# Performance work log

Measured on AMD Instinct MI355X. Metric: run time of the kernel, lower is better.

The kernel has to match this reference:

```python
import jax, jax.numpy as jnp
import numpy as np

DIV_VAL = 11.313708498984761  # sqrt(128), the softmax temperature used as div_val


def setup_inputs() -> dict:
    key = jax.random.key(0)
    kq, kk, kv = jax.random.split(key, 3)
    B, Lq, Lk, D = 16, 4096, 4096, 128
    return {
        "query": jax.random.normal(kq, (B, Lq, D), dtype=jnp.float32),
        "key": jax.random.normal(kk, (B, Lk, D), dtype=jnp.float32),
        "value": jax.random.normal(kv, (B, Lk, D), dtype=jnp.float32),
    }


def reference(query, key, value):
    # qk = Q @ K^T, scaled by 1/div_val  -> [B, Lq, Lk]
    scaled_qk = jnp.einsum("bqd,bkd->bqk", query, key) / DIV_VAL
    # numerically stable softmax over last axis; dropout is identity (eval / p=0)
    attn = jax.nn.softmax(scaled_qk, axis=-1)
    # output = attn @ V -> [B, Lq, Dv]
    return jnp.einsum("bqk,bkd->bqd", attn, value)
```

## Files before the change

### kernel.cpp

```cpp
#include <hip/hip_runtime.h>

#define B_  16
#define L_  4096
#define D_  128
#define NT  (L_ / 64)

typedef __attribute__((ext_vector_type(8)))  __bf16 bf16x8;
typedef __attribute__((ext_vector_type(2)))  __bf16 bf16x2;
typedef __attribute__((ext_vector_type(16))) float  f32x16;
typedef __attribute__((ext_vector_type(4)))  float  f32x4;
typedef __attribute__((ext_vector_type(4)))  int    i32x4;
typedef __attribute__((ext_vector_type(8)))  unsigned short u16x8;
typedef __attribute__((ext_vector_type(4)))  unsigned short u16x4;

#ifndef __has_builtin
#define __has_builtin(x) 0
#endif
#if __has_builtin(__builtin_amdgcn_permlane32_swap)
#define HAVE_PLSWAP 1
#else
#define HAVE_PLSWAP 0
#endif

__device__ __forceinline__ unsigned short f2bf(float f){
  unsigned u = __builtin_bit_cast(unsigned, f);
  u += 0x7fffu + ((u >> 16) & 1u);
  return (unsigned short)(u >> 16);
}

__device__ __forceinline__ int packbf(float a, float b){
  bf16x2 t; t[0] = (__bf16)a; t[1] = (__bf16)b;
  return __builtin_bit_cast(int, t);
}

__device__ __forceinline__ void gload16(const void* g, void* l){
  __builtin_amdgcn_global_load_lds(
      (const __attribute__((address_space(1))) unsigned int*)g,
      (__attribute__((address_space(3))) unsigned int*)l, 16, 0, 0);
}

__device__ __forceinline__ f32x16 z16(){
  f32x16 t;
#pragma unroll
  for (int i = 0; i < 16; ++i) t[i] = 0.f;
  return t;
}

__global__ void cvt_bf16_kernel(const float* __restrict__ in,
                                unsigned short* __restrict__ out, int n8,
                                float scale){
  int i = blockIdx.x * blockDim.x + threadIdx.x;
  if (i >= n8) return;
  const float4* p = reinterpret_cast<const float4*>(in) + (size_t)i * 2;
  float4 a = p[0], b = p[1];
  u16x8 o;
  o[0]=f2bf(a.x*scale); o[1]=f2bf(a.y*scale); o[2]=f2bf(a.z*scale); o[3]=f2bf(a.w*scale);
  o[4]=f2bf(b.x*scale); o[5]=f2bf(b.y*scale); o[6]=f2bf(b.z*scale); o[7]=f2bf(b.w*scale);
  reinterpret_cast<u16x8*>(out)[i] = o;
}

__global__ void transpose_v_kernel(const float* __restrict__ V,
                                   unsigned short* __restrict__ Vt){
  __shared__ unsigned short tile[64][65];
  const int k0 = blockIdx.x * 64, d0 = blockIdx.y * 64, b = blockIdx.z;
  const int tr = threadIdx.x >> 4, tc = threadIdx.x & 15;
  const float* src = V + ((size_t)b * L_ + k0) * D_ + d0;
#pragma unroll
  for (int p = 0; p < 4; ++p){
    int kl = p * 16 + tr;
    float4 v = *reinterpret_cast<const float4*>(src + (size_t)kl * D_ + tc * 4);
    tile[kl][tc*4+0] = f2bf(v.x);
    tile[kl][tc*4+1] = f2bf(v.y);
    tile[kl][tc*4+2] = f2bf(v.z);
    tile[kl][tc*4+3] = f2bf(v.w);
  }
  __syncthreads();
  unsigned short* dst = Vt + (size_t)b * D_ * L_ + (size_t)d0 * L_ + k0;
#pragma unroll
  for (int p = 0; p < 4; ++p){
    int dl = p * 16 + tr;
    u16x4 o;
    o[0] = tile[tc*4+0][dl];
    o[1] = tile[tc*4+1][dl];
    o[2] = tile[tc*4+2][dl];
    o[3] = tile[tc*4+3][dl];
    *reinterpret_cast<u16x4*>(dst + (size_t)dl * L_ + tc * 4) = o;
  }
}

__device__ __forceinline__ bf16x8 mkchunk(float a0,float a1,float a2,float a3,
                                          float a4,float a5,float a6,float a7,
                                          int hi){
  int x0 = packbf(a0,a1), x1 = packbf(a2,a3);
  int x2 = packbf(a4,a5), x3 = packbf(a6,a7);
  int W0, W1, W2, W3;
#if HAVE_PLSWAP
  {
    auto r = __builtin_amdgcn_permlane32_swap((unsigned)x0, (unsigned)x2, false, false);
    W0 = (int)r[0]; W2 = (int)r[1];
  }
  {
    auto r = __builtin_amdgcn_permlane32_swap((unsigned)x1, (unsigned)x3, false, false);
    W1 = (int)r[0]; W3 = (int)r[1];
  }
  (void)hi;
#else
  int y0 = __shfl_xor(x0, 32), y1 = __shfl_xor(x1, 32);
  int y2 = __shfl_xor(x2, 32), y3 = __shfl_xor(x3, 32);
  W0 = hi ? y2 : x0;  W1 = hi ? y3 : x1;
  W2 = hi ? x2 : y0;  W3 = hi ? x3 : y1;
#endif
  i32x4 ww; ww[0]=W0; ww[1]=W1; ww[2]=W2; ww[3]=W3;
  return __builtin_bit_cast(bf16x8, ww);
}

__global__ __launch_bounds__(512, 1)
void attn_kernel(const float* __restrict__ Q,
                 const unsigned short* __restrict__ Kb,
                 const unsigned short* __restrict__ Vt,
                 float* __restrict__ out){
  __shared__ char smem[131072];
  char* Klds = smem;
  char* Vlds = smem + 65536;

  const int tid = threadIdx.x;
  const int w = tid >> 6, l = tid & 63;
  const int row = l & 31, hi = l >> 5;
  const int swz = (row & 15) << 4;
  const int b = blockIdx.x, qt = blockIdx.y;

  const float* qptr = Q + ((size_t)b * L_ + (size_t)qt * 256 + w * 32 + row) * D_;
  bf16x8 qf[8];
#pragma unroll
  for (int c = 0; c < 8; ++c){
    float4 a  = *reinterpret_cast<const float4*>(qptr + c * 16 + hi * 8);
    float4 bb = *reinterpret_cast<const float4*>(qptr + c * 16 + hi * 8 + 4);
    u16x8 o;
    o[0]=f2bf(a.x);  o[1]=f2bf(a.y);  o[2]=f2bf(a.z);  o[3]=f2bf(a.w);
    o[4]=f2bf(bb.x); o[5]=f2bf(bb.y); o[6]=f2bf(bb.z); o[7]=f2bf(bb.w);
    qf[c] = __builtin_bit_cast(bf16x8, o);
  }

  const char* Kg = (const char*)(Kb + (size_t)b * L_ * D_);
  const char* Vg = (const char*)(Vt + (size_t)b * (size_t)D_ * L_);

  f32x16 o[4];
#pragma unroll
  for (int n = 0; n < 4; ++n) o[n] = z16();
  float ln = 0.f;

  auto STAGE = [&](int bsel, int t){
    char* kd = Klds + bsel * 16384;
    char* vd = Vlds + bsel * 16384;
    const int kv0 = t * 64;
#pragma unroll
    for (int j = 0; j < 2; ++j){
      int idx = j * 512 + tid;
      int kr = idx >> 4, sc = idx & 15;
      int clog = (sc << 4) ^ ((kr & 15) << 4);
      gload16(Kg + (size_t)(kv0 + kr) * 256 + clog, kd + idx * 16);
    }
#pragma unroll
    for (int j = 0; j < 2; ++j){
      int idx = j * 512 + tid;
      int lr = idx >> 4, sc = idx & 15;
      int clog = (sc << 4) ^ ((lr & 15) << 4);
      int dd = lr + ((clog >> 7) << 6);
      gload16(Vg + (size_t)dd * (L_ * 2) + (size_t)kv0 * 2 + (clog & 127),
              vd + idx * 16);
    }
  };

#define QKT(C0, C1, KC)                                                        \
  {                                                                            \
    const char* Kc_ = (KC);                                                    \
    C0 = z16(); C1 = z16();                                                    \
    __builtin_amdgcn_s_setprio(1);                                             \
    _Pragma("unroll")                                                          \
    for (int c = 0; c < 8; ++c){                                               \
      bf16x8 kf0 = *(const bf16x8*)(Kc_ + row * 256 + ((c*32 + hi*16) ^ swz)); \
      bf16x8 kf1 = *(const bf16x8*)(Kc_ + (row+32) * 256 + ((c*32 + hi*16) ^ swz)); \
      C0 = __builtin_amdgcn_mfma_f32_32x32x16_bf16(kf0, qf[c], C0, 0, 0, 0);   \
      C1 = __builtin_amdgcn_mfma_f32_32x32x16_bf16(kf1, qf[c], C1, 0, 0, 0);   \
    }                                                                          \
    __builtin_amdgcn_s_setprio(0);                                             \
  }

#define SMPACK(P0, P1)                                                         \
    _Pragma("unroll")                                                          \
    for (int i2 = 0; i2 < 16; ++i2){                                           \
      P0[i2] = __builtin_amdgcn_exp2f(P0[i2]);                                 \
      P1[i2] = __builtin_amdgcn_exp2f(P1[i2]);                                 \
    }                                                                          \
    {                                                                          \
      f32x16 pt_ = P0 + P1;                                                    \
      float a0 = pt_[0]+pt_[1],  a1 = pt_[2]+pt_[3];                           \
      float a2 = pt_[4]+pt_[5],  a3 = pt_[6]+pt_[7];                           \
      float a4 = pt_[8]+pt_[9],  a5 = pt_[10]+pt_[11];                         \
      float a6 = pt_[12]+pt_[13], a7 = pt_[14]+pt_[15];                        \
      ln += ((a0+a1)+(a2+a3)) + ((a4+a5)+(a6+a7));                             \
    }                                                                          \
    bf16x8 pa0 = mkchunk(P0[0],P0[1],P0[2],P0[3],P0[4],P0[5],P0[6],P0[7], hi); \
    bf16x8 pa1 = mkchunk(P0[8],P0[9],P0[10],P0[11],P0[12],P0[13],P0[14],P0[15], hi); \
    bf16x8 pa2 = mkchunk(P1[0],P1[1],P1[2],P1[3],P1[4],P1[5],P1[6],P1[7], hi); \
    bf16x8 pa3 = mkchunk(P1[8],P1[9],P1[10],P1[11],P1[12],P1[13],P1[14],P1[15], hi);

#define VF(VP, N, CH)                                                          \
  (*(const bf16x8*)((VP) + ((N & 1) * 32 + row) * 256 +                        \
                    ((((N >> 1) * 128) + (CH)*32 + hi*16) ^ swz)))

#define PVONLY(VP)                                                             \
  {                                                                            \
    const char* Vp_ = (VP);                                                    \
    __builtin_amdgcn_s_setprio(1);                                             \
    _Pragma("unroll")                                                          \
    for (int n2 = 0; n2 < 4; ++n2){                                            \
      bf16x8 vf0 = VF(Vp_, n2, 0);                                             \
      bf16x8 vf1 = VF(Vp_, n2, 1);                                             \
      bf16x8 vf2 = VF(Vp_, n2, 2);                                             \
      bf16x8 vf3 = VF(Vp_, n2, 3);                                             \
      o[n2] = __builtin_amdgcn_mfma_f32_32x32x16_bf16(vf0, pa0, o[n2], 0,0,0); \
      o[n2] = __builtin_amdgcn_mfma_f32_32x32x16_bf16(vf1, pa1, o[n2], 0,0,0); \
      o[n2] = __builtin_amdgcn_mfma_f32_32x32x16_bf16(vf2, pa2, o[n2], 0,0,0); \
      o[n2] = __builtin_amdgcn_mfma_f32_32x32x16_bf16(vf3, pa3, o[n2], 0,0,0); \
    }                                                                          \
    __builtin_amdgcn_s_setprio(0);                                             \
  }

#define BODY(I, C0, C1, P0, P1)                                                \
  {                                                                            \
    const int i_ = (I);                                                        \
    if (i_ + 2 < NT) STAGE((i_ + 2) & 3, i_ + 2);                              \
    SMPACK(P0, P1)                                                             \
    const char* Kc_ = Klds + (i_ & 3) * 16384;                                 \
    const char* Vp_ = Vlds + ((i_ - 1) & 3) * 16384;                           \
    C0 = z16(); C1 = z16();                                                    \
    __builtin_amdgcn_s_setprio(1);                                             \
    _Pragma("unroll")                                                          \
    for (int c = 0; c < 4; ++c){                                               \
      bf16x8 kf0a = *(const bf16x8*)(Kc_ + row * 256 + (((2*c)*32 + hi*16) ^ swz)); \
      bf16x8 kf1a = *(const bf16x8*)(Kc_ + (row+32) * 256 + (((2*c)*32 + hi*16) ^ swz)); \
      bf16x8 kf0b = *(const bf16x8*)(Kc_ + row * 256 + (((2*c+1)*32 + hi*16) ^ swz)); \
      bf16x8 kf1b = *(const bf16x8*)(Kc_ + (row+32) * 256 + (((2*c+1)*32 + hi*16) ^ swz)); \
      bf16x8 vf0 = VF(Vp_, c, 0);                                              \
      bf16x8 vf1 = VF(Vp_, c, 1);                                              \
      bf16x8 vf2 = VF(Vp_, c, 2);                                              \
      bf16x8 vf3 = VF(Vp_, c, 3);                                              \
      C0 = __builtin_amdgcn_mfma_f32_32x32x16_bf16(kf0a, qf[2*c],   C0, 0,0,0);\
      o[c] = __builtin_amdgcn_mfma_f32_32x32x16_bf16(vf0, pa0, o[c], 0,0,0);   \
      C1 = __builtin_amdgcn_mfma_f32_32x32x16_bf16(kf1a, qf[2*c],   C1, 0,0,0);\
      o[c] = __builtin_amdgcn_mfma_f32_32x32x16_bf16(vf1, pa1, o[c], 0,0,0);   \
      C0 = __builtin_amdgcn_mfma_f32_32x32x16_bf16(kf0b, qf[2*c+1], C0, 0,0,0);\
      o[c] = __builtin_amdgcn_mfma_f32_32x32x16_bf16(vf2, pa2, o[c], 0,0,0);   \
      C1 = __builtin_amdgcn_mfma_f32_32x32x16_bf16(kf1b, qf[2*c+1], C1, 0,0,0);\
      o[c] = __builtin_amdgcn_mfma_f32_32x32x16_bf16(vf3, pa3, o[c], 0,0,0);   \
    }                                                                          \
    __builtin_amdgcn_s_setprio(0);                                             \
    if (i_ + 2 < NT) { asm volatile("s_waitcnt vmcnt(4)" ::: "memory"); }      \
    else             { asm volatile("s_waitcnt vmcnt(0)" ::: "memory"); }      \
    __builtin_amdgcn_s_barrier();                                              \
  }

  STAGE(0, 0); STAGE(1, 1); STAGE(2, 2);
  asm volatile("s_waitcnt vmcnt(4)" ::: "memory");
  __builtin_amdgcn_s_barrier();

  f32x16 sA0, sA1, sB0, sB1;
  QKT(sA0, sA1, Klds);

  for (int i = 1; i <= NT - 3; i += 2){
    BODY(i,     sB0, sB1, sA0, sA1);
    BODY(i + 1, sA0, sA1, sB0, sB1);
  }
  BODY(NT - 1, sB0, sB1, sA0, sA1);
  { SMPACK(sB0, sB1) PVONLY(Vlds + ((NT - 1) & 3) * 16384); }

  float lt = ln + __shfl_xor(ln, 32);
  float inv = 1.0f / lt;
  float* outp = out + ((size_t)b * L_ + (size_t)qt * 256 + w * 32 + row) * D_;
#pragma unroll
  for (int n = 0; n < 4; ++n)
#pragma unroll
    for (int rq = 0; rq < 4; ++rq){
      f32x4 v4;
      v4[0] = o[n][rq*4+0] * inv;
      v4[1] = o[n][rq*4+1] * inv;
      v4[2] = o[n][rq*4+2] * inv;
      v4[3] = o[n][rq*4+3] * inv;
      *reinterpret_cast<f32x4*>(outp + n * 32 + rq * 8 + hi * 4) = v4;
    }
}

extern "C" void kernel_launch(void* const* d_in, const int* in_sizes, int n_in,
                              void* d_out, int out_size, void* d_ws, size_t ws_size,
                              hipStream_t stream){
  const float* Q = (const float*)d_in[0];
  const float* K = (const float*)d_in[1];
  const float* V = (const float*)d_in[2];
  float* out = (float*)d_out;

  const size_t NE = (size_t)B_ * L_ * D_;
  unsigned short* kb = (unsigned short*)d_ws;
  unsigned short* vt = kb + NE;

  const float SCALE_L2E = 1.4426950408889634f / 11.313708498984761f;
  int n8 = (int)(NE / 8);
  cvt_bf16_kernel<<<dim3(n8 / 256), 256, 0, stream>>>(K, kb, n8, SCALE_L2E);
  transpose_v_kernel<<<dim3(L_ / 64, D_ / 64, B_), 256, 0, stream>>>(V, vt);
  attn_kernel<<<dim3(B_, L_ / 256), 512, 0, stream>>>(Q, kb, vt, out);
}
```

Measured before the change: 172.3 us.

## Split each KV tile across two wave groups and reduce partial outputs via LDS

Doubles the block to 1024 threads. Two groups of eight waves share the same query rows, and each group handles half of every 64-key tile (32 keys), so each wave does half the QK^T and PV MFMA work per tile. Partial outputs and row sums are combined through shared memory at the end using extra barriers. The aim is more waves per CU to hide latency, at the cost of duplicated Q registers, a final reduction pass, and more barrier overhead per tile.

```diff
diff --git a/kernel.cpp b/kernel.cpp
--- a/kernel.cpp
+++ b/kernel.cpp
@@ -114,7 +114,7 @@
   return __builtin_bit_cast(bf16x8, ww);
 }
 
-__global__ __launch_bounds__(512, 1)
+__global__ __launch_bounds__(1024, 1)
 void attn_kernel(const float* __restrict__ Q,
                  const unsigned short* __restrict__ Kb,
                  const unsigned short* __restrict__ Vt,
@@ -125,11 +125,12 @@
 
   const int tid = threadIdx.x;
   const int w = tid >> 6, l = tid & 63;
+  const int wq = w & 7, wg = w >> 3;
   const int row = l & 31, hi = l >> 5;
   const int swz = (row & 15) << 4;
   const int b = blockIdx.x, qt = blockIdx.y;
 
-  const float* qptr = Q + ((size_t)b * L_ + (size_t)qt * 256 + w * 32 + row) * D_;
+  const float* qptr = Q + ((size_t)b * L_ + (size_t)qt * 256 + wq * 32 + row) * D_;
   bf16x8 qf[8];
 #pragma unroll
   for (int c = 0; c < 8; ++c){
@@ -153,61 +154,50 @@
     char* kd = Klds + bsel * 16384;
     char* vd = Vlds + bsel * 16384;
     const int kv0 = t * 64;
-#pragma unroll
-    for (int j = 0; j < 2; ++j){
-      int idx = j * 512 + tid;
-      int kr = idx >> 4, sc = idx & 15;
+    {
+      int kr = tid >> 4, sc = tid & 15;
       int clog = (sc << 4) ^ ((kr & 15) << 4);
-      gload16(Kg + (size_t)(kv0 + kr) * 256 + clog, kd + idx * 16);
-    }
-#pragma unroll
-    for (int j = 0; j < 2; ++j){
-      int idx = j * 512 + tid;
-      int lr = idx >> 4, sc = idx & 15;
+      gload16(Kg + (size_t)(kv0 + kr) * 256 + clog, kd + tid * 16);
+    }
+    {
+      int lr = tid >> 4, sc = tid & 15;
       int clog = (sc << 4) ^ ((lr & 15) << 4);
       int dd = lr + ((clog >> 7) << 6);
       gload16(Vg + (size_t)dd * (L_ * 2) + (size_t)kv0 * 2 + (clog & 127),
-              vd + idx * 16);
+              vd + tid * 16);
     }
   };
 
-#define QKT(C0, C1, KC)                                                        \
+#define QKT(C0, KC)                                                            \
   {                                                                            \
     const char* Kc_ = (KC);                                                    \
-    C0 = z16(); C1 = z16();                                                    \
+    C0 = z16();                                                                \
     __builtin_amdgcn_s_setprio(1);                                             \
     _Pragma("unroll")                                                          \
     for (int c = 0; c < 8; ++c){                                               \
-      bf16x8 kf0 = *(const bf16x8*)(Kc_ + row * 256 + ((c*32 + hi*16) ^ swz)); \
-      bf16x8 kf1 = *(const bf16x8*)(Kc_ + (row+32) * 256 + ((c*32 + hi*16) ^ swz)); \
-      C0 = __builtin_amdgcn_mfma_f32_32x32x16_bf16(kf0, qf[c], C0, 0, 0, 0);   \
-      C1 = __builtin_amdgcn_mfma_f32_32x32x16_bf16(kf1, qf[c], C1, 0, 0, 0);   \
+      bf16x8 kf = *(const bf16x8*)(Kc_ + (wg * 32 + row) * 256 +               \
+                                   ((c*32 + hi*16) ^ swz));                    \
+      C0 = __builtin_amdgcn_mfma_f32_32x32x16_bf16(kf, qf[c], C0, 0, 0, 0);    \
     }                                                                          \
     __builtin_amdgcn_s_setprio(0);                                             \
   }
 
-#define SMPACK(P0, P1)                                                         \
+#define SMPACK(P0)                                                             \
     _Pragma("unroll")                                                          \
-    for (int i2 = 0; i2 < 16; ++i2){                                           \
-      P0[i2] = __builtin_amdgcn_exp2f(P0[i2]);                                 \
-      P1[i2] = __builtin_amdgcn_exp2f(P1[i2]);                                 \
-    }                                                                          \
+    for (int i2 = 0; i2 < 16; ++i2) P0[i2] = __builtin_amdgcn_exp2f(P0[i2]);   \
     {                                                                          \
-      f32x16 pt_ = P0 + P1;                                                    \
-      float a0 = pt_[0]+pt_[1],  a1 = pt_[2]+pt_[3];                           \
-      float a2 = pt_[4]+pt_[5],  a3 = pt_[6]+pt_[7];                           \
-      float a4 = pt_[8]+pt_[9],  a5 = pt_[10]+pt_[11];                         \
-      float a6 = pt_[12]+pt_[13], a7 = pt_[14]+pt_[15];                        \
+      float a0 = P0[0]+P0[1],  a1 = P0[2]+P0[3];                               \
+      float a2 = P0[4]+P0[5],  a3 = P0[6]+P0[7];                               \
+      float a4 = P0[8]+P0[9],  a5 = P0[10]+P0[11];                             \
+      float a6 = P0[12]+P0[13], a7 = P0[14]+P0[15];                            \
       ln += ((a0+a1)+(a2+a3)) + ((a4+a5)+(a6+a7));                             \
     }                                                                          \
     bf16x8 pa0 = mkchunk(P0[0],P0[1],P0[2],P0[3],P0[4],P0[5],P0[6],P0[7], hi); \
-    bf16x8 pa1 = mkchunk(P0[8],P0[9],P0[10],P0[11],P0[12],P0[13],P0[14],P0[15], hi); \
-    bf16x8 pa2 = mkchunk(P1[0],P1[1],P1[2],P1[3],P1[4],P1[5],P1[6],P1[7], hi); \
-    bf16x8 pa3 = mkchunk(P1[8],P1[9],P1[10],P1[11],P1[12],P1[13],P1[14],P1[15], hi);
+    bf16x8 pa1 = mkchunk(P0[8],P0[9],P0[10],P0[11],P0[12],P0[13],P0[14],P0[15], hi);
 
 #define VF(VP, N, CH)                                                          \
   (*(const bf16x8*)((VP) + ((N & 1) * 32 + row) * 256 +                        \
-                    ((((N >> 1) * 128) + (CH)*32 + hi*16) ^ swz)))
+                    ((((N >> 1) * 128) + (wg * 2 + (CH)) * 32 + hi*16) ^ swz)))
 
 #define PVONLY(VP)                                                             \
   {                                                                            \
@@ -217,78 +207,114 @@
     for (int n2 = 0; n2 < 4; ++n2){                                            \
       bf16x8 vf0 = VF(Vp_, n2, 0);                                             \
       bf16x8 vf1 = VF(Vp_, n2, 1);                                             \
-      bf16x8 vf2 = VF(Vp_, n2, 2);                                             \
-      bf16x8 vf3 = VF(Vp_, n2, 3);                                             \
       o[n2] = __builtin_amdgcn_mfma_f32_32x32x16_bf16(vf0, pa0, o[n2], 0,0,0); \
       o[n2] = __builtin_amdgcn_mfma_f32_32x32x16_bf16(vf1, pa1, o[n2], 0,0,0); \
-      o[n2] = __builtin_amdgcn_mfma_f32_32x32x16_bf16(vf2, pa2, o[n2], 0,0,0); \
-      o[n2] = __builtin_amdgcn_mfma_f32_32x32x16_bf16(vf3, pa3, o[n2], 0,0,0); \
     }                                                                          \
     __builtin_amdgcn_s_setprio(0);                                             \
   }
 
-#define BODY(I, C0, C1, P0, P1)                                                \
+#define BODY(I, C0, P0)                                                        \
   {                                                                            \
     const int i_ = (I);                                                        \
     if (i_ + 2 < NT) STAGE((i_ + 2) & 3, i_ + 2);                              \
-    SMPACK(P0, P1)                                                             \
+    SMPACK(P0)                                                                 \
     const char* Kc_ = Klds + (i_ & 3) * 16384;                                 \
     const char* Vp_ = Vlds + ((i_ - 1) & 3) * 16384;                           \
-    C0 = z16(); C1 = z16();                                                    \
+    C0 = z16();                                                                \
     __builtin_amdgcn_s_setprio(1);                                             \
     _Pragma("unroll")                                                          \
     for (int c = 0; c < 4; ++c){                                               \
-      bf16x8 kf0a = *(const bf16x8*)(Kc_ + row * 256 + (((2*c)*32 + hi*16) ^ swz)); \
-      bf16x8 kf1a = *(const bf16x8*)(Kc_ + (row+32) * 256 + (((2*c)*32 + hi*16) ^ swz)); \
-      bf16x8 kf0b = *(const bf16x8*)(Kc_ + row * 256 + (((2*c+1)*32 + hi*16) ^ swz)); \
-      bf16x8 kf1b = *(const bf16x8*)(Kc_ + (row+32) * 256 + (((2*c+1)*32 + hi*16) ^ swz)); \
+      bf16x8 kfa = *(const bf16x8*)(Kc_ + (wg * 32 + row) * 256 +              \
+                                    (((2*c)*32 + hi*16) ^ swz));               \
+      bf16x8 kfb = *(const bf16x8*)(Kc_ + (wg * 32 + row) * 256 +              \
+                                    (((2*c+1)*32 + hi*16) ^ swz));             \
       bf16x8 vf0 = VF(Vp_, c, 0);                                              \
       bf16x8 vf1 = VF(Vp_, c, 1);                                              \
-      bf16x8 vf2 = VF(Vp_, c, 2);                                              \
-      bf16x8 vf3 = VF(Vp_, c, 3);                                              \
-      C0 = __builtin_amdgcn_mfma_f32_32x32x16_bf16(kf0a, qf[2*c],   C0, 0,0,0);\
+      C0 = __builtin_amdgcn_mfma_f32_32x32x16_bf16(kfa, qf[2*c],   C0, 0,0,0); \
       o[c] = __builtin_amdgcn_mfma_f32_32x32x16_bf16(vf0, pa0, o[c], 0,0,0);   \
-      C1 = __builtin_amdgcn_mfma_f32_32x32x16_bf16(kf1a, qf[2*c],   C1, 0,0,0);\
+      C0 = __builtin_amdgcn_mfma_f32_32x32x16_bf16(kfb, qf[2*c+1], C0, 0,0,0); \
       o[c] = __builtin_amdgcn_mfma_f32_32x32x16_bf16(vf1, pa1, o[c], 0,0,0);   \
-      C0 = __builtin_amdgcn_mfma_f32_32x32x16_bf16(kf0b, qf[2*c+1], C0, 0,0,0);\
-      o[c] = __builtin_amdgcn_mfma_f32_32x32x16_bf16(vf2, pa2, o[c], 0,0,0);   \
-      C1 = __builtin_amdgcn_mfma_f32_32x32x16_bf16(kf1b, qf[2*c+1], C1, 0,0,0);\
-      o[c] = __builtin_amdgcn_mfma_f32_32x32x16_bf16(vf3, pa3, o[c], 0,0,0);   \
     }                                                                          \
     __builtin_amdgcn_s_setprio(0);                                             \
-    if (i_ + 2 < NT) { asm volatile("s_waitcnt vmcnt(4)" ::: "memory"); }      \
+    if (i_ + 2 < NT) { asm volatile("s_waitcnt vmcnt(2)" ::: "memory"); }      \
     else             { asm volatile("s_waitcnt vmcnt(0)" ::: "memory"); }      \
     __builtin_amdgcn_s_barrier();                                              \
   }
 
   STAGE(0, 0); STAGE(1, 1); STAGE(2, 2);
-  asm volatile("s_waitcnt vmcnt(4)" ::: "memory");
+  asm volatile("s_waitcnt vmcnt(2)" ::: "memory");
   __builtin_amdgcn_s_barrier();
 
-  f32x16 sA0, sA1, sB0, sB1;
-  QKT(sA0, sA1, Klds);
+  f32x16 sA, sB;
+  QKT(sA, Klds);
 
   for (int i = 1; i <= NT - 3; i += 2){
-    BODY(i,     sB0, sB1, sA0, sA1);
-    BODY(i + 1, sA0, sA1, sB0, sB1);
-  }
-  BODY(NT - 1, sB0, sB1, sA0, sA1);
-  { SMPACK(sB0, sB1) PVONLY(Vlds + ((NT - 1) & 3) * 16384); }
-
-  float lt = ln + __shfl_xor(ln, 32);
-  float inv = 1.0f / lt;
-  float* outp = out + ((size_t)b * L_ + (size_t)qt * 256 + w * 32 + row) * D_;
-#pragma unroll
-  for (int n = 0; n < 4; ++n)
-#pragma unroll
-    for (int rq = 0; rq < 4; ++rq){
-      f32x4 v4;
-      v4[0] = o[n][rq*4+0] * inv;
-      v4[1] = o[n][rq*4+1] * inv;
-      v4[2] = o[n][rq*4+2] * inv;
-      v4[3] = o[n][rq*4+3] * inv;
-      *reinterpret_cast<f32x4*>(outp + n * 32 + rq * 8 + hi * 4) = v4;
-    }
+    BODY(i,     sB, sA);
+    BODY(i + 1, sA, sB);
+  }
+  BODY(NT - 1, sB, sA);
+  { SMPACK(sB) PVONLY(Vlds + ((NT - 1) & 3) * 16384); }
+
+  __syncthreads();
+  float* lnbuf = (float*)(smem + 65536);
+  float4* xbuf = (float4*)smem;
+  const int slot = wq * 64 + l;
+
+  if (wg == 1){
+#pragma unroll
+    for (int c = 0; c < 4; ++c){
+      f32x4 q0; q0[0]=o[0][c*4+0]; q0[1]=o[0][c*4+1]; q0[2]=o[0][c*4+2]; q0[3]=o[0][c*4+3];
+      xbuf[c * 512 + slot] = *(float4*)&q0;
+      f32x4 q1; q1[0]=o[1][c*4+0]; q1[1]=o[1][c*4+1]; q1[2]=o[1][c*4+2]; q1[3]=o[1][c*4+3];
+      xbuf[(4 + c) * 512 + slot] = *(float4*)&q1;
+    }
+    lnbuf[slot] = ln;
+  }
+  __syncthreads();
+  if (wg == 0){
+#pragma unroll
+    for (int c = 0; c < 4; ++c){
+      float4 q0 = xbuf[c * 512 + slot];
+      o[0][c*4+0]+=q0.x; o[0][c*4+1]+=q0.y; o[0][c*4+2]+=q0.z; o[0][c*4+3]+=q0.w;
+      float4 q1 = xbuf[(4 + c) * 512 + slot];
+      o[1][c*4+0]+=q1.x; o[1][c*4+1]+=q1.y; o[1][c*4+2]+=q1.z; o[1][c*4+3]+=q1.w;
+    }
+    ln += lnbuf[slot];
+  }
+  __syncthreads();
+  if (wg == 1){
+#pragma unroll
+    for (int c = 0; c < 4; ++c){
+      f32x4 q0; q0[0]=o[2][c*4+0]; q0[1]=o[2][c*4+1]; q0[2]=o[2][c*4+2]; q0[3]=o[2][c*4+3];
+      xbuf[c * 512 + slot] = *(float4*)&q0;
+      f32x4 q1; q1[0]=o[3][c*4+0]; q1[1]=o[3][c*4+1]; q1[2]=o[3][c*4+2]; q1[3]=o[3][c*4+3];
+      xbuf[(4 + c) * 512 + slot] = *(float4*)&q1;
+    }
+  }
+  __syncthreads();
+  if (wg == 0){
+#pragma unroll
+    for (int c = 0; c < 4; ++c){
+      float4 q0 = xbuf[c * 512 + slot];
+      o[2][c*4+0]+=q0.x; o[2][c*4+1]+=q0.y; o[2][c*4+2]+=q0.z; o[2][c*4+3]+=q0.w;
+      float4 q1 = xbuf[(4 + c) * 512 + slot];
+      o[3][c*4+0]+=q1.x; o[3][c*4+1]+=q1.y; o[3][c*4+2]+=q1.z; o[3][c*4+3]+=q1.w;
+    }
+    float lt = ln + __shfl_xor(ln, 32);
+    float inv = 1.0f / lt;
+    float* outp = out + ((size_t)b * L_ + (size_t)qt * 256 + wq * 32 + row) * D_;
+#pragma unroll
+    for (int n = 0; n < 4; ++n)
+#pragma unroll
+      for (int rq = 0; rq < 4; ++rq){
+        f32x4 v4;
+        v4[0] = o[n][rq*4+0] * inv;
+        v4[1] = o[n][rq*4+1] * inv;
+        v4[2] = o[n][rq*4+2] * inv;
+        v4[3] = o[n][rq*4+3] * inv;
+        *reinterpret_cast<f32x4*>(outp + n * 32 + rq * 8 + hi * 4) = v4;
+      }
+  }
 }
 
 extern "C" void kernel_launch(void* const* d_in, const int* in_sizes, int n_in,
@@ -307,5 +333,5 @@
   int n8 = (int)(NE / 8);
   cvt_bf16_kernel<<<dim3(n8 / 256), 256, 0, stream>>>(K, kb, n8, SCALE_L2E);
   transpose_v_kernel<<<dim3(L_ / 64, D_ / 64, B_), 256, 0, stream>>>(V, vt);
-  attn_kernel<<<dim3(B_, L_ / 256), 512, 0, stream>>>(Q, kb, vt, out);
-}
+  attn_kernel<<<dim3(B_, L_ / 256), 1024, 0, stream>>>(Q, kb, vt, out);
+}
```

Result: slower. 655.4 us (+280.3%).

## Switch to 128-key double-buffered tiles with sequential QK/PV per half

Applied to the files above, without the earlier changes.

Replaces the 4-deep, 64-key ring of staged K/V tiles and the software-pipelined loop body, which interleaved QK^T of tile i with PV of tile i-1, with a 2-buffer, 128-key tile loop. Each iteration computes QK^T for both 64-key halves, then softmax-pack and PV for each half, and waits on all loads before the barrier. The V LDS layout is also simplified to plain row-major d-rows with an XOR swizzle. The aim is to cut the number of barriers and per-tile overhead. In exchange it loses the MFMA interleaving of the two matmuls and the deeper prefetch, which can expose memory latency.

```diff
diff --git a/kernel.cpp b/kernel.cpp
--- a/kernel.cpp
+++ b/kernel.cpp
@@ -3,7 +3,7 @@
 #define B_  16
 #define L_  4096
 #define D_  128
-#define NT  (L_ / 64)
+#define NT2 (L_ / 128)
 
 typedef __attribute__((ext_vector_type(8)))  __bf16 bf16x8;
 typedef __attribute__((ext_vector_type(2)))  __bf16 bf16x2;
@@ -150,36 +150,36 @@
   float ln = 0.f;
 
   auto STAGE = [&](int bsel, int t){
-    char* kd = Klds + bsel * 16384;
-    char* vd = Vlds + bsel * 16384;
-    const int kv0 = t * 64;
-#pragma unroll
-    for (int j = 0; j < 2; ++j){
+    char* kd = Klds + bsel * 32768;
+    char* vd = Vlds + bsel * 32768;
+    const int kv0 = t * 128;
+#pragma unroll
+    for (int j = 0; j < 4; ++j){
       int idx = j * 512 + tid;
       int kr = idx >> 4, sc = idx & 15;
       int clog = (sc << 4) ^ ((kr & 15) << 4);
       gload16(Kg + (size_t)(kv0 + kr) * 256 + clog, kd + idx * 16);
     }
 #pragma unroll
-    for (int j = 0; j < 2; ++j){
+    for (int j = 0; j < 4; ++j){
       int idx = j * 512 + tid;
-      int lr = idx >> 4, sc = idx & 15;
-      int clog = (sc << 4) ^ ((lr & 15) << 4);
-      int dd = lr + ((clog >> 7) << 6);
-      gload16(Vg + (size_t)dd * (L_ * 2) + (size_t)kv0 * 2 + (clog & 127),
-              vd + idx * 16);
+      int dr = idx >> 4, sc = idx & 15;
+      int clog = (sc << 4) ^ ((dr & 15) << 4);
+      gload16(Vg + (size_t)dr * (L_ * 2) + (size_t)kv0 * 2 + clog, vd + idx * 16);
     }
   };
 
-#define QKT(C0, C1, KC)                                                        \
+#define QKTH(C0, C1, KC, H)                                                    \
   {                                                                            \
     const char* Kc_ = (KC);                                                    \
     C0 = z16(); C1 = z16();                                                    \
     __builtin_amdgcn_s_setprio(1);                                             \
     _Pragma("unroll")                                                          \
     for (int c = 0; c < 8; ++c){                                               \
-      bf16x8 kf0 = *(const bf16x8*)(Kc_ + row * 256 + ((c*32 + hi*16) ^ swz)); \
-      bf16x8 kf1 = *(const bf16x8*)(Kc_ + (row+32) * 256 + ((c*32 + hi*16) ^ swz)); \
+      bf16x8 kf0 = *(const bf16x8*)(Kc_ + ((H)*64 + row) * 256 +               \
+                                    ((c*32 + hi*16) ^ swz));                   \
+      bf16x8 kf1 = *(const bf16x8*)(Kc_ + ((H)*64 + row + 32) * 256 +          \
+                                    ((c*32 + hi*16) ^ swz));                   \
       C0 = __builtin_amdgcn_mfma_f32_32x32x16_bf16(kf0, qf[c], C0, 0, 0, 0);   \
       C1 = __builtin_amdgcn_mfma_f32_32x32x16_bf16(kf1, qf[c], C1, 0, 0, 0);   \
     }                                                                          \
@@ -205,20 +205,17 @@
     bf16x8 pa2 = mkchunk(P1[0],P1[1],P1[2],P1[3],P1[4],P1[5],P1[6],P1[7], hi); \
     bf16x8 pa3 = mkchunk(P1[8],P1[9],P1[10],P1[11],P1[12],P1[13],P1[14],P1[15], hi);
 
-#define VF(VP, N, CH)                                                          \
-  (*(const bf16x8*)((VP) + ((N & 1) * 32 + row) * 256 +                        \
-                    ((((N >> 1) * 128) + (CH)*32 + hi*16) ^ swz)))
-
-#define PVONLY(VP)                                                             \
+#define PVH(VP, H)                                                             \
   {                                                                            \
     const char* Vp_ = (VP);                                                    \
     __builtin_amdgcn_s_setprio(1);                                             \
     _Pragma("unroll")                                                          \
     for (int n2 = 0; n2 < 4; ++n2){                                            \
-      bf16x8 vf0 = VF(Vp_, n2, 0);                                             \
-      bf16x8 vf1 = VF(Vp_, n2, 1);                                             \
-      bf16x8 vf2 = VF(Vp_, n2, 2);                                             \
-      bf16x8 vf3 = VF(Vp_, n2, 3);                                             \
+      const char* vr_ = Vp_ + (n2 * 32 + row) * 256;                           \
+      bf16x8 vf0 = *(const bf16x8*)(vr_ + ((((H)*4+0)*32 + hi*16) ^ swz));     \
+      bf16x8 vf1 = *(const bf16x8*)(vr_ + ((((H)*4+1)*32 + hi*16) ^ swz));     \
+      bf16x8 vf2 = *(const bf16x8*)(vr_ + ((((H)*4+2)*32 + hi*16) ^ swz));     \
+      bf16x8 vf3 = *(const bf16x8*)(vr_ + ((((H)*4+3)*32 + hi*16) ^ swz));     \
       o[n2] = __builtin_amdgcn_mfma_f32_32x32x16_bf16(vf0, pa0, o[n2], 0,0,0); \
       o[n2] = __builtin_amdgcn_mfma_f32_32x32x16_bf16(vf1, pa1, o[n2], 0,0,0); \
       o[n2] = __builtin_amdgcn_mfma_f32_32x32x16_bf16(vf2, pa2, o[n2], 0,0,0); \
@@ -227,53 +224,27 @@
     __builtin_amdgcn_s_setprio(0);                                             \
   }
 
-#define BODY(I, C0, C1, P0, P1)                                                \
-  {                                                                            \
-    const int i_ = (I);                                                        \
-    if (i_ + 2 < NT) STAGE((i_ + 2) & 3, i_ + 2);                              \
-    SMPACK(P0, P1)                                                             \
-    const char* Kc_ = Klds + (i_ & 3) * 16384;                                 \
-    const char* Vp_ = Vlds + ((i_ - 1) & 3) * 16384;                           \
-    C0 = z16(); C1 = z16();                                                    \
-    __builtin_amdgcn_s_setprio(1);                                             \
-    _Pragma("unroll")                                                          \
-    for (int c = 0; c < 4; ++c){                                               \
-      bf16x8 kf0a = *(const bf16x8*)(Kc_ + row * 256 + (((2*c)*32 + hi*16) ^ swz)); \
-      bf16x8 kf1a = *(const bf16x8*)(Kc_ + (row+32) * 256 + (((2*c)*32 + hi*16) ^ swz)); \
-      bf16x8 kf0b = *(const bf16x8*)(Kc_ + row * 256 + (((2*c+1)*32 + hi*16) ^ swz)); \
-      bf16x8 kf1b = *(const bf16x8*)(Kc_ + (row+32) * 256 + (((2*c+1)*32 + hi*16) ^ swz)); \
-      bf16x8 vf0 = VF(Vp_, c, 0);                                              \
-      bf16x8 vf1 = VF(Vp_, c, 1);                                              \
-      bf16x8 vf2 = VF(Vp_, c, 2);                                              \
-      bf16x8 vf3 = VF(Vp_, c, 3);                                              \
-      C0 = __builtin_amdgcn_mfma_f32_32x32x16_bf16(kf0a, qf[2*c],   C0, 0,0,0);\
-      o[c] = __builtin_amdgcn_mfma_f32_32x32x16_bf16(vf0, pa0, o[c], 0,0,0);   \
-      C1 = __builtin_amdgcn_mfma_f32_32x32x16_bf16(kf1a, qf[2*c],   C1, 0,0,0);\
-      o[c] = __builtin_amdgcn_mfma_f32_32x32x16_bf16(vf1, pa1, o[c], 0,0,0);   \
-      C0 = __builtin_amdgcn_mfma_f32_32x32x16_bf16(kf0b, qf[2*c+1], C0, 0,0,0);\
-      o[c] = __builtin_amdgcn_mfma_f32_32x32x16_bf16(vf2, pa2, o[c], 0,0,0);   \
-      C1 = __builtin_amdgcn_mfma_f32_32x32x16_bf16(kf1b, qf[2*c+1], C1, 0,0,0);\
-      o[c] = __builtin_amdgcn_mfma_f32_32x32x16_bf16(vf3, pa3, o[c], 0,0,0);   \
-    }                                                                          \
-    __builtin_amdgcn_s_setprio(0);                                             \
-    if (i_ + 2 < NT) { asm volatile("s_waitcnt vmcnt(4)" ::: "memory"); }      \
-    else             { asm volatile("s_waitcnt vmcnt(0)" ::: "memory"); }      \
-    __builtin_amdgcn_s_barrier();                                              \
-  }
-
-  STAGE(0, 0); STAGE(1, 1); STAGE(2, 2);
-  asm volatile("s_waitcnt vmcnt(4)" ::: "memory");
+  STAGE(0, 0);
+  asm volatile("s_waitcnt vmcnt(0)" ::: "memory");
   __builtin_amdgcn_s_barrier();
+  int cur = 0;
 
   f32x16 sA0, sA1, sB0, sB1;
-  QKT(sA0, sA1, Klds);
-
-  for (int i = 1; i <= NT - 3; i += 2){
-    BODY(i,     sB0, sB1, sA0, sA1);
-    BODY(i + 1, sA0, sA1, sB0, sB1);
-  }
-  BODY(NT - 1, sB0, sB1, sA0, sA1);
-  { SMPACK(sB0, sB1) PVONLY(Vlds + ((NT - 1) & 3) * 16384); }
+  for (int i = 0; i < NT2; ++i){
+    if (i + 1 < NT2) STAGE(cur ^ 1, i + 1);
+
+    const char* Kc = Klds + cur * 32768;
+    const char* Vc = Vlds + cur * 32768;
+
+    QKTH(sA0, sA1, Kc, 0);
+    QKTH(sB0, sB1, Kc, 1);
+    { SMPACK(sA0, sA1) PVH(Vc, 0) }
+    { SMPACK(sB0, sB1) PVH(Vc, 1) }
+
+    asm volatile("s_waitcnt vmcnt(0)" ::: "memory");
+    __builtin_amdgcn_s_barrier();
+    cur ^= 1;
+  }
 
   float lt = ln + __shfl_xor(ln, 32);
   float inv = 1.0f / lt;
```

Measured after the change: 172.6 us. Within noise of the previous version (+0.2%).

## Load K tiles directly from global into registers, dropping K LDS staging

Applied to the files above, without the earlier changes.

K is no longer staged through shared memory. Each wave now loads its 64-row K tile from global memory straight into registers at the start of every iteration, which halves the LDS footprint. The V staging call moves to the end of the loop body, and the explicit vmcnt waits are removed, so the code relies on the compiler's own waits for the register loads. The aim is to cut LDS traffic and barrier-bound staging. In exchange, every wave re-reads the same K tile from global memory or L2, global load latency sits right before the QK MFMAs, and register pressure grows by 16 bf16x8 values per lane.

```diff
diff --git a/kernel.cpp b/kernel.cpp
--- a/kernel.cpp
+++ b/kernel.cpp
@@ -119,9 +119,8 @@
                  const unsigned short* __restrict__ Kb,
                  const unsigned short* __restrict__ Vt,
                  float* __restrict__ out){
-  __shared__ char smem[131072];
-  char* Klds = smem;
-  char* Vlds = smem + 65536;
+  __shared__ char smem[65536];
+  char* Vlds = smem;
 
   const int tid = threadIdx.x;
   const int w = tid >> 6, l = tid & 63;
@@ -150,16 +149,8 @@
   float ln = 0.f;
 
   auto STAGE = [&](int bsel, int t){
-    char* kd = Klds + bsel * 16384;
     char* vd = Vlds + bsel * 16384;
     const int kv0 = t * 64;
-#pragma unroll
-    for (int j = 0; j < 2; ++j){
-      int idx = j * 512 + tid;
-      int kr = idx >> 4, sc = idx & 15;
-      int clog = (sc << 4) ^ ((kr & 15) << 4);
-      gload16(Kg + (size_t)(kv0 + kr) * 256 + clog, kd + idx * 16);
-    }
 #pragma unroll
     for (int j = 0; j < 2; ++j){
       int idx = j * 512 + tid;
@@ -171,20 +162,13 @@
     }
   };
 
-#define QKT(C0, C1, KC)                                                        \
-  {                                                                            \
-    const char* Kc_ = (KC);                                                    \
-    C0 = z16(); C1 = z16();                                                    \
-    __builtin_amdgcn_s_setprio(1);                                             \
-    _Pragma("unroll")                                                          \
-    for (int c = 0; c < 8; ++c){                                               \
-      bf16x8 kf0 = *(const bf16x8*)(Kc_ + row * 256 + ((c*32 + hi*16) ^ swz)); \
-      bf16x8 kf1 = *(const bf16x8*)(Kc_ + (row+32) * 256 + ((c*32 + hi*16) ^ swz)); \
-      C0 = __builtin_amdgcn_mfma_f32_32x32x16_bf16(kf0, qf[c], C0, 0, 0, 0);   \
-      C1 = __builtin_amdgcn_mfma_f32_32x32x16_bf16(kf1, qf[c], C1, 0, 0, 0);   \
-    }                                                                          \
-    __builtin_amdgcn_s_setprio(0);                                             \
-  }
+#define KLOAD(I)                                                               \
+    const char* k0p_ = Kg + ((size_t)(I) * 64 + row) * 256 + hi * 16;          \
+    bf16x8 kfa[8], kfb[8];                                                     \
+    _Pragma("unroll")                                                          \
+    for (int c = 0; c < 8; ++c) kfa[c] = *(const bf16x8*)(k0p_ + c * 32);      \
+    _Pragma("unroll")                                                          \
+    for (int c = 0; c < 8; ++c) kfb[c] = *(const bf16x8*)(k0p_ + 32*256 + c*32);
 
 #define SMPACK(P0, P1)                                                         \
     _Pragma("unroll")                                                          \
@@ -230,43 +214,47 @@
 #define BODY(I, C0, C1, P0, P1)                                                \
   {                                                                            \
     const int i_ = (I);                                                        \
-    if (i_ + 2 < NT) STAGE((i_ + 2) & 3, i_ + 2);                              \
+    KLOAD(i_)                                                                  \
     SMPACK(P0, P1)                                                             \
-    const char* Kc_ = Klds + (i_ & 3) * 16384;                                 \
     const char* Vp_ = Vlds + ((i_ - 1) & 3) * 16384;                           \
     C0 = z16(); C1 = z16();                                                    \
     __builtin_amdgcn_s_setprio(1);                                             \
     _Pragma("unroll")                                                          \
     for (int c = 0; c < 4; ++c){                                               \
-      bf16x8 kf0a = *(const bf16x8*)(Kc_ + row * 256 + (((2*c)*32 + hi*16) ^ swz)); \
-      bf16x8 kf1a = *(const bf16x8*)(Kc_ + (row+32) * 256 + (((2*c)*32 + hi*16) ^ swz)); \
-      bf16x8 kf0b = *(const bf16x8*)(Kc_ + row * 256 + (((2*c+1)*32 + hi*16) ^ swz)); \
-      bf16x8 kf1b = *(const bf16x8*)(Kc_ + (row+32) * 256 + (((2*c+1)*32 + hi*16) ^ swz)); \
       bf16x8 vf0 = VF(Vp_, c, 0);                                              \
       bf16x8 vf1 = VF(Vp_, c, 1);                                              \
       bf16x8 vf2 = VF(Vp_, c, 2);                                              \
       bf16x8 vf3 = VF(Vp_, c, 3);                                              \
-      C0 = __builtin_amdgcn_mfma_f32_32x32x16_bf16(kf0a, qf[2*c],   C0, 0,0,0);\
+      C0 = __builtin_amdgcn_mfma_f32_32x32x16_bf16(kfa[2*c],   qf[2*c],   C0, 0,0,0); \
       o[c] = __builtin_amdgcn_mfma_f32_32x32x16_bf16(vf0, pa0, o[c], 0,0,0);   \
-      C1 = __builtin_amdgcn_mfma_f32_32x32x16_bf16(kf1a, qf[2*c],   C1, 0,0,0);\
+      C1 = __builtin_amdgcn_mfma_f32_32x32x16_bf16(kfb[2*c],   qf[2*c],   C1, 0,0,0); \
       o[c] = __builtin_amdgcn_mfma_f32_32x32x16_bf16(vf1, pa1, o[c], 0,0,0);   \
-      C0 = __builtin_amdgcn_mfma_f32_32x32x16_bf16(kf0b, qf[2*c+1], C0, 0,0,0);\
+      C0 = __builtin_amdgcn_mfma_f32_32x32x16_bf16(kfa[2*c+1], qf[2*c+1], C0, 0,0,0); \
       o[c] = __builtin_amdgcn_mfma_f32_32x32x16_bf16(vf2, pa2, o[c], 0,0,0);   \
-      C1 = __builtin_amdgcn_mfma_f32_32x32x16_bf16(kf1b, qf[2*c+1], C1, 0,0,0);\
+      C1 = __builtin_amdgcn_mfma_f32_32x32x16_bf16(kfb[2*c+1], qf[2*c+1], C1, 0,0,0); \
       o[c] = __builtin_amdgcn_mfma_f32_32x32x16_bf16(vf3, pa3, o[c], 0,0,0);   \
     }                                                                          \
     __builtin_amdgcn_s_setprio(0);                                             \
-    if (i_ + 2 < NT) { asm volatile("s_waitcnt vmcnt(4)" ::: "memory"); }      \
-    else             { asm volatile("s_waitcnt vmcnt(0)" ::: "memory"); }      \
+    if (i_ + 2 < NT) STAGE((i_ + 2) & 3, i_ + 2);                              \
     __builtin_amdgcn_s_barrier();                                              \
   }
 
   STAGE(0, 0); STAGE(1, 1); STAGE(2, 2);
-  asm volatile("s_waitcnt vmcnt(4)" ::: "memory");
+  asm volatile("s_waitcnt vmcnt(0)" ::: "memory");
   __builtin_amdgcn_s_barrier();
 
   f32x16 sA0, sA1, sB0, sB1;
-  QKT(sA0, sA1, Klds);
+  {
+    KLOAD(0)
+    sA0 = z16(); sA1 = z16();
+    __builtin_amdgcn_s_setprio(1);
+#pragma unroll
+    for (int c = 0; c < 8; ++c){
+      sA0 = __builtin_amdgcn_mfma_f32_32x32x16_bf16(kfa[c], qf[c], sA0, 0, 0, 0);
+      sA1 = __builtin_amdgcn_mfma_f32_32x32x16_bf16(kfb[c], qf[c], sA1, 0, 0, 0);
+    }
+    __builtin_amdgcn_s_setprio(0);
+  }
 
   for (int i = 1; i <= NT - 3; i += 2){
     BODY(i,     sB0, sB1, sA0, sA1);
```

Result: slower. 441.2 us (+156.0%).
